# Optimization experiments

Hardware: AMD Instinct MI355X
Metric: run time of the kernel (lower is better)

The kernel has to match this reference:

```python
import jax, jax.numpy as jnp
import numpy as np

IN_FEATURES = 512
OUT_FEATURES = 256
N = 2048

def setup_inputs() -> dict:
    key = jax.random.key(0)
    k1, k2, k3 = jax.random.split(key, 3)
    x = jax.random.normal(k1, (N, IN_FEATURES), dtype=jnp.float32)
    # kaiming_uniform_(a=sqrt(5)) -> uniform(-b, b) with b = sqrt(6/((1+5)*fan_in)) = 1/sqrt(fan_in)
    bound_w = 1.0 / np.sqrt(IN_FEATURES)
    weight = jax.random.uniform(k2, (OUT_FEATURES, IN_FEATURES), dtype=jnp.float32,
                                minval=-bound_w, maxval=bound_w)
    bound_b = 1.0 / np.sqrt(IN_FEATURES)
    bias = jax.random.uniform(k3, (OUT_FEATURES,), dtype=jnp.float32,
                              minval=-bound_b, maxval=bound_b)
    return {"x": x, "weight": weight, "bias": bias}

def reference(x, weight, bias):
    # MAM fully-connected (beta == 0 path):
    # prod[n, k, j] = x[n, k] * weight[j, k]
    # C[n, j] = max_k prod[n,k,j] + min_k prod[n,k,j] + bias[j]
    prod = x[:, :, None] * weight.T[None, :, :]   # [N, in, out]
    C = jnp.max(prod, axis=1) + jnp.min(prod, axis=1) + bias[None, :]
    return C
```

## Files before the change

kernel.cpp:

```cpp
#include <hip/hip_runtime.h>
#include <math.h>

#define N_ 2048
#define K_ 512
#define J_ 256
#define KC 64
#define NPW 16

typedef float f32x16 __attribute__((ext_vector_type(16)));

#define MAX3(acc, a, b) asm("v_max3_f32 %0, %0, %1, %2" : "+v"(acc) : "v"(a), "v"(b))
#define MIN3(acc, a, b) asm("v_min3_f32 %0, %0, %1, %2" : "+v"(acc) : "v"(a), "v"(b))

__global__ __launch_bounds__(512, 4) void mam_fused5(
    const float* __restrict__ x, const float* __restrict__ w,
    const float* __restrict__ bias, float* __restrict__ out)
{
    __shared__ float cmb[8][NPW][128];

    const int t    = threadIdx.x;
    const int lane = t & 63;
    const int kc   = __builtin_amdgcn_readfirstlane(t >> 6);

    const int wg0 = (int)blockIdx.x;
    const int wg  = (wg0 & 7) * 64 + (wg0 >> 3);
    const int jb  = wg & 3;
    const int ng  = wg >> 2;

    const int j   = jb * 64 + lane;
    const int n0  = ng * NPW;

    float4 wreg[16];
    {
        const float4* wp = (const float4*)(w + (size_t)j * K_ + kc * KC);
#pragma unroll
        for (int i = 0; i < 16; ++i) wreg[i] = wp[i];
    }

    const float* xb = x + (size_t)n0 * K_ + kc * KC;

    float mxv[NPW], mnv[NPW];
#pragma unroll
    for (int n = 0; n < NPW; ++n) { mxv[n] = -__builtin_inff(); mnv[n] = __builtin_inff(); }

#pragma unroll
    for (int n = 0; n < NPW; ++n) {
        f32x16 xv[4];
        asm volatile(
            "s_load_dwordx16 %0, %4, %5\n\t"
            "s_load_dwordx16 %1, %4, %6\n\t"
            "s_load_dwordx16 %2, %4, %7\n\t"
            "s_load_dwordx16 %3, %4, %8\n\t"
            "s_waitcnt lgkmcnt(0)"
            : "=&s"(xv[0]), "=&s"(xv[1]), "=&s"(xv[2]), "=&s"(xv[3])
            : "s"(xb), "i"(n * 2048 + 0), "i"(n * 2048 + 64),
              "i"(n * 2048 + 128), "i"(n * 2048 + 192));
#pragma unroll
        for (int i = 0; i < 16; ++i) {
            const float p0 = wreg[i].x * xv[i >> 2][(i & 3) * 4 + 0];
            const float p1 = wreg[i].y * xv[i >> 2][(i & 3) * 4 + 1];
            const float p2 = wreg[i].z * xv[i >> 2][(i & 3) * 4 + 2];
            const float p3 = wreg[i].w * xv[i >> 2][(i & 3) * 4 + 3];
            MAX3(mxv[n], p0, p1); MAX3(mxv[n], p2, p3);
            MIN3(mnv[n], p0, p1); MIN3(mnv[n], p2, p3);
        }
    }

#pragma unroll
    for (int n = 0; n < NPW; ++n) {
        cmb[kc][n][lane]      = mxv[n];
        cmb[kc][n][64 + lane] = mnv[n];
    }
    __syncthreads();

    const float bj = bias[j];
#pragma unroll
    for (int u = 0; u < 2; ++u) {
        const int n = kc * 2 + u;
        float a = cmb[0][n][lane];
        float b = cmb[0][n][64 + lane];
#pragma unroll
        for (int c = 1; c < 8; ++c) {
            a = fmaxf(a, cmb[c][n][lane]);
            b = fminf(b, cmb[c][n][64 + lane]);
        }
        out[(size_t)(n0 + n) * J_ + j] = a + b + bj;
    }
}

extern "C" void kernel_launch(void* const* d_in, const int* in_sizes, int n_in,
                              void* d_out, int out_size, void* d_ws, size_t ws_size,
                              hipStream_t stream) {
    const float* x    = (const float*)d_in[0];
    const float* w    = (const float*)d_in[1];
    const float* bias = (const float*)d_in[2];
    float* out = (float*)d_out;

    dim3 grid(512);
    mam_fused5<<<grid, 512, 0, stream>>>(x, w, bias, out);
}
```

Baseline: 73.90 us.

## Retile so each block covers all outputs for 4 rows, staging x in LDS

Each block now handles 4 rows of x and all 256 output columns. Each wave owns a 64-wide K slice and streams the weights from global in 8-column sub-chunks, while the x rows are staged into LDS through direct global-to-LDS loads. This replaces the earlier 16-row by 64-column tiling that held weights in registers and read x through scalar loads. The weights are now reread from global/L2 by every block, and each weight load waits on vmcnt(0) before computing, which may expose latency. The LDS reduction buffer also grows to 64KB, which may limit occupancy.

```diff
diff --git a/kernel.cpp b/kernel.cpp
--- a/kernel.cpp
+++ b/kernel.cpp
@@ -4,87 +4,119 @@
 #define N_ 2048
 #define K_ 512
 #define J_ 256
-#define KC 64
-#define NPW 16
+#define NR 4
 
-typedef float f32x16 __attribute__((ext_vector_type(16)));
+typedef __attribute__((address_space(3))) float       lds_f;
+typedef const __attribute__((address_space(1))) float glb_f;
 
 #define MAX3(acc, a, b) asm("v_max3_f32 %0, %0, %1, %2" : "+v"(acc) : "v"(a), "v"(b))
 #define MIN3(acc, a, b) asm("v_min3_f32 %0, %0, %1, %2" : "+v"(acc) : "v"(a), "v"(b))
 
-__global__ __launch_bounds__(512, 4) void mam_fused5(
+__global__ __launch_bounds__(512, 4) void mam_fused7(
     const float* __restrict__ x, const float* __restrict__ w,
     const float* __restrict__ bias, float* __restrict__ out)
 {
-    __shared__ float cmb[8][NPW][128];
+    __shared__ __align__(16) float xls[NR * 512];
+    __shared__ __align__(16) float cmb[8 * NR * J_ * 2];
 
     const int t    = threadIdx.x;
     const int lane = t & 63;
     const int kc   = __builtin_amdgcn_readfirstlane(t >> 6);
+    const int n0   = (int)blockIdx.x * NR;
 
-    const int wg0 = (int)blockIdx.x;
-    const int wg  = (wg0 & 7) * 64 + (wg0 >> 3);
-    const int jb  = wg & 3;
-    const int ng  = wg >> 2;
-
-    const int j   = jb * 64 + lane;
-    const int n0  = ng * NPW;
-
-    float4 wreg[16];
     {
-        const float4* wp = (const float4*)(w + (size_t)j * K_ + kc * KC);
-#pragma unroll
-        for (int i = 0; i < 16; ++i) wreg[i] = wp[i];
+        const int r = kc >> 1, h = kc & 1;
+        __builtin_amdgcn_global_load_lds(
+            (glb_f*)(x + (size_t)(n0 + r) * K_ + h * 256 + lane * 4),
+            (lds_f*)(xls + r * 512 + h * 256), 16, 0, 0);
     }
 
-    const float* xb = x + (size_t)n0 * K_ + kc * KC;
+    const float* wq[4];
+#pragma unroll
+    for (int q = 0; q < 4; ++q)
+        wq[q] = w + (size_t)(q * 64 + lane) * K_ + kc * 64;
 
-    float mxv[NPW], mnv[NPW];
+    float mx[NR][4], mn[NR][4];
 #pragma unroll
-    for (int n = 0; n < NPW; ++n) { mxv[n] = -__builtin_inff(); mnv[n] = __builtin_inff(); }
+    for (int n = 0; n < NR; ++n)
+#pragma unroll
+        for (int q = 0; q < 4; ++q) {
+            mx[n][q] = -__builtin_inff();
+            mn[n][q] =  __builtin_inff();
+        }
+
+    __syncthreads();
+
+    float4 wv[4][2];
+
+#define WLOAD(S0, S1)                                                         \
+    asm volatile(                                                             \
+        "global_load_dwordx4 %0, %8, off offset:" S0 "\n\t"                   \
+        "global_load_dwordx4 %1, %8, off offset:" S1 "\n\t"                   \
+        "global_load_dwordx4 %2, %9, off offset:" S0 "\n\t"                   \
+        "global_load_dwordx4 %3, %9, off offset:" S1 "\n\t"                   \
+        "global_load_dwordx4 %4, %10, off offset:" S0 "\n\t"                  \
+        "global_load_dwordx4 %5, %10, off offset:" S1 "\n\t"                  \
+        "global_load_dwordx4 %6, %11, off offset:" S0 "\n\t"                  \
+        "global_load_dwordx4 %7, %11, off offset:" S1 "\n\t"                  \
+        "s_waitcnt vmcnt(0)"                                                  \
+        : "=&v"(wv[0][0]), "=&v"(wv[0][1]), "=&v"(wv[1][0]), "=&v"(wv[1][1]), \
+          "=&v"(wv[2][0]), "=&v"(wv[2][1]), "=&v"(wv[3][0]), "=&v"(wv[3][1])  \
+        : "v"(wq[0]), "v"(wq[1]), "v"(wq[2]), "v"(wq[3]))
+
+#define CSUB(S)                                                               \
+    _Pragma("unroll")                                                         \
+    for (int n = 0; n < NR; ++n) {                                            \
+        const float4 x0 = *(const float4*)&xls[n * 512 + kc * 64 + (S) * 8];  \
+        const float4 x1 = *(const float4*)&xls[n * 512 + kc * 64 + (S) * 8 + 4]; \
+        _Pragma("unroll")                                                     \
+        for (int q = 0; q < 4; ++q) {                                         \
+            const float4 a0 = wv[q][0], a1 = wv[q][1];                        \
+            const float p0 = x0.x * a0.x, p1 = x0.y * a0.y;                   \
+            const float p2 = x0.z * a0.z, p3 = x0.w * a0.w;                   \
+            const float p4 = x1.x * a1.x, p5 = x1.y * a1.y;                   \
+            const float p6 = x1.z * a1.z, p7 = x1.w * a1.w;                   \
+            MAX3(mx[n][q], p0, p1); MAX3(mx[n][q], p2, p3);                   \
+            MAX3(mx[n][q], p4, p5); MAX3(mx[n][q], p6, p7);                   \
+            MIN3(mn[n][q], p0, p1); MIN3(mn[n][q], p2, p3);                   \
+            MIN3(mn[n][q], p4, p5); MIN3(mn[n][q], p6, p7);                   \
+        }                                                                     \
+    }
+
+    WLOAD(  "0",  "16"); CSUB(0);
+    WLOAD( "32",  "48"); CSUB(1);
+    WLOAD( "64",  "80"); CSUB(2);
+    WLOAD( "96", "112"); CSUB(3);
+    WLOAD("128", "144"); CSUB(4);
+    WLOAD("160", "176"); CSUB(5);
+    WLOAD("192", "208"); CSUB(6);
+    WLOAD("224", "240"); CSUB(7);
+
+#undef WLOAD
+#undef CSUB
 
 #pragma unroll
-    for (int n = 0; n < NPW; ++n) {
-        f32x16 xv[4];
-        asm volatile(
-            "s_load_dwordx16 %0, %4, %5\n\t"
-            "s_load_dwordx16 %1, %4, %6\n\t"
-            "s_load_dwordx16 %2, %4, %7\n\t"
-            "s_load_dwordx16 %3, %4, %8\n\t"
-            "s_waitcnt lgkmcnt(0)"
-            : "=&s"(xv[0]), "=&s"(xv[1]), "=&s"(xv[2]), "=&s"(xv[3])
-            : "s"(xb), "i"(n * 2048 + 0), "i"(n * 2048 + 64),
-              "i"(n * 2048 + 128), "i"(n * 2048 + 192));
+    for (int n = 0; n < NR; ++n)
 #pragma unroll
-        for (int i = 0; i < 16; ++i) {
-            const float p0 = wreg[i].x * xv[i >> 2][(i & 3) * 4 + 0];
-            const float p1 = wreg[i].y * xv[i >> 2][(i & 3) * 4 + 1];
-            const float p2 = wreg[i].z * xv[i >> 2][(i & 3) * 4 + 2];
-            const float p3 = wreg[i].w * xv[i >> 2][(i & 3) * 4 + 3];
-            MAX3(mxv[n], p0, p1); MAX3(mxv[n], p2, p3);
-            MIN3(mnv[n], p0, p1); MIN3(mnv[n], p2, p3);
+        for (int q = 0; q < 4; ++q) {
+            float2 v; v.x = mx[n][q]; v.y = mn[n][q];
+            *(float2*)&cmb[((kc * NR + n) * J_ + q * 64 + lane) * 2] = v;
         }
-    }
+    __syncthreads();
 
 #pragma unroll
-    for (int n = 0; n < NPW; ++n) {
-        cmb[kc][n][lane]      = mxv[n];
-        cmb[kc][n][64 + lane] = mnv[n];
-    }
-    __syncthreads();
-
-    const float bj = bias[j];
+    for (int i = 0; i < 2; ++i) {
+        const int u = t + i * 512;
+        const int n = u >> 8;
+        const int j = u & 255;
+        float a = -__builtin_inff(), b = __builtin_inff();
 #pragma unroll
-    for (int u = 0; u < 2; ++u) {
-        const int n = kc * 2 + u;
-        float a = cmb[0][n][lane];
-        float b = cmb[0][n][64 + lane];
-#pragma unroll
-        for (int c = 1; c < 8; ++c) {
-            a = fmaxf(a, cmb[c][n][lane]);
-            b = fminf(b, cmb[c][n][64 + lane]);
+        for (int c = 0; c < 8; ++c) {
+            const float2 p = *(const float2*)&cmb[((c * NR + n) * J_ + j) * 2];
+            a = fmaxf(a, p.x);
+            b = fminf(b, p.y);
         }
-        out[(size_t)(n0 + n) * J_ + j] = a + b + bj;
+        out[(size_t)(n0 + n) * J_ + j] = a + b + bias[j];
     }
 }
 
@@ -96,6 +128,6 @@
     const float* bias = (const float*)d_in[2];
     float* out = (float*)d_out;
 
-    dim3 grid(512);
-    mam_fused5<<<grid, 512, 0, stream>>>(x, w, bias, out);
+    dim3 grid(N_ / NR);
+    mam_fused7<<<grid, 512, 0, stream>>>(x, w, bias, out);
 }
```

Result: slower. 91.91 us (+24.4%).

## Retile max-min FC into 64x8 LDS register blocks with staged global loads

Applied to the files above, without the earlier changes.

Replaces the per-wave scalar-load scheme (each lane holds one weight column and streams x rows through SGPRs) with a 64-row by 8-column output tile per block. Four waves each handle a 128-wide K slice, staging x and w chunks through padded LDS, and each lane computes a 4x2 register tile. The next chunk's global loads are issued before the current chunk's compute to overlap latency. This trades SGPR broadcast loads for LDS reads with 2D register reuse and changes the grid to 1024 blocks of 256 threads. The risks are LDS bandwidth and bank-conflict cost, and WRITES overwriting LDS that other lanes may still be reading, since each wave appears to touch only its own region.

```diff
diff --git a/kernel.cpp b/kernel.cpp
--- a/kernel.cpp
+++ b/kernel.cpp
@@ -4,87 +4,143 @@
 #define N_ 2048
 #define K_ 512
 #define J_ 256
-#define KC 64
-#define NPW 16
 
-typedef float f32x16 __attribute__((ext_vector_type(16)));
+typedef float f32x4 __attribute__((ext_vector_type(4)));
+typedef float f32x2 __attribute__((ext_vector_type(2)));
+typedef __attribute__((address_space(3))) float  lds_f;
+typedef __attribute__((address_space(3))) f32x4  lds_f4;
 
 #define MAX3(acc, a, b) asm("v_max3_f32 %0, %0, %1, %2" : "+v"(acc) : "v"(a), "v"(b))
 #define MIN3(acc, a, b) asm("v_min3_f32 %0, %0, %1, %2" : "+v"(acc) : "v"(a), "v"(b))
 
-__global__ __launch_bounds__(512, 4) void mam_fused5(
+__global__ __launch_bounds__(256, 4) void mam_fused8(
     const float* __restrict__ x, const float* __restrict__ w,
     const float* __restrict__ bias, float* __restrict__ out)
 {
-    __shared__ float cmb[8][NPW][128];
+    __shared__ __align__(16) float sm[9856];
 
     const int t    = threadIdx.x;
     const int lane = t & 63;
-    const int kc   = __builtin_amdgcn_readfirstlane(t >> 6);
+    const int ks   = __builtin_amdgcn_readfirstlane(t >> 6);
 
     const int wg0 = (int)blockIdx.x;
-    const int wg  = (wg0 & 7) * 64 + (wg0 >> 3);
-    const int jb  = wg & 3;
-    const int ng  = wg >> 2;
+    const int wg  = (wg0 & 7) * 128 + (wg0 >> 3);
+    const int bx  = wg & 31;
+    const int by  = wg >> 5;
+    const int j0  = bx * 8;
+    const int n0  = by * 64;
 
-    const int j   = jb * 64 + lane;
-    const int n0  = ng * NPW;
+    const int rg = lane >> 2;
+    const int cg = lane & 3;
 
-    float4 wreg[16];
-    {
-        const float4* wp = (const float4*)(w + (size_t)j * K_ + kc * KC);
+    const int XB = ks * 2176;
+    const int WB = 8704 + ks * 288;
+
+    const float* xsb = x + (size_t)n0 * K_ + ks * 128;
+    const float* wsb = w + (size_t)j0 * K_ + ks * 128;
+
+    unsigned vxo[8];
 #pragma unroll
-        for (int i = 0; i < 16; ++i) wreg[i] = wp[i];
+    for (int m = 0; m < 8; ++m)
+        vxo[m] = (unsigned)((lane >> 3) * 2048 + (lane & 7) * 16 + m * 16384);
+    const unsigned vwo = (unsigned)((lane >> 3) * 2048 + (lane & 7) * 16);
+
+    lds_f* xwp = (lds_f*)&sm[XB] + (lane >> 4) * 68 + ((lane >> 3) & 1) * 32 + (lane & 7) * 4;
+    lds_f* wwp = (lds_f*)&sm[WB] + (lane >> 3) * 36 + (lane & 7) * 4;
+
+    float mx[4][2], mn[4][2];
+#pragma unroll
+    for (int i = 0; i < 4; ++i)
+#pragma unroll
+        for (int jj = 0; jj < 2; ++jj) {
+            mx[i][jj] = -__builtin_inff();
+            mn[i][jj] =  __builtin_inff();
+        }
+
+    f32x4 px[8], pw;
+
+#define LOADS(OFS)                                                            \
+    asm volatile(                                                             \
+        "global_load_dwordx4 %0, %9, %17 offset:" OFS "\n\t"                  \
+        "global_load_dwordx4 %1, %10, %17 offset:" OFS "\n\t"                 \
+        "global_load_dwordx4 %2, %11, %17 offset:" OFS "\n\t"                 \
+        "global_load_dwordx4 %3, %12, %17 offset:" OFS "\n\t"                 \
+        "global_load_dwordx4 %4, %13, %17 offset:" OFS "\n\t"                 \
+        "global_load_dwordx4 %5, %14, %17 offset:" OFS "\n\t"                 \
+        "global_load_dwordx4 %6, %15, %17 offset:" OFS "\n\t"                 \
+        "global_load_dwordx4 %7, %16, %17 offset:" OFS "\n\t"                 \
+        "global_load_dwordx4 %8, %18, %19 offset:" OFS                        \
+        : "=&v"(px[0]), "=&v"(px[1]), "=&v"(px[2]), "=&v"(px[3]),             \
+          "=&v"(px[4]), "=&v"(px[5]), "=&v"(px[6]), "=&v"(px[7]), "=&v"(pw)   \
+        : "v"(vxo[0]), "v"(vxo[1]), "v"(vxo[2]), "v"(vxo[3]),                 \
+          "v"(vxo[4]), "v"(vxo[5]), "v"(vxo[6]), "v"(vxo[7]),                 \
+          "s"(xsb), "v"(vwo), "s"(wsb))
+
+#define WRITES()                                                              \
+    {                                                                         \
+        asm volatile("s_waitcnt vmcnt(0)" ::: "memory");                      \
+        _Pragma("unroll")                                                     \
+        for (int m = 0; m < 8; ++m)                                           \
+            *(lds_f4*)(xwp + m * 272) = px[m];                                \
+        *(lds_f4*)wwp = pw;                                                   \
     }
 
-    const float* xb = x + (size_t)n0 * K_ + kc * KC;
+#define COMPUTE()                                                             \
+    _Pragma("unroll")                                                         \
+    for (int q = 0; q < 8; ++q) {                                             \
+        f32x4 xv[4], wv[2];                                                   \
+        _Pragma("unroll")                                                     \
+        for (int i = 0; i < 4; ++i)                                           \
+            xv[i] = *(const f32x4*)&sm[XB + ((rg >> 1) + 8 * i) * 68          \
+                                       + (rg & 1) * 32 + q * 4];              \
+        _Pragma("unroll")                                                     \
+        for (int jj = 0; jj < 2; ++jj)                                        \
+            wv[jj] = *(const f32x4*)&sm[WB + (cg * 2 + jj) * 36 + q * 4];     \
+        _Pragma("unroll")                                                     \
+        for (int i = 0; i < 4; ++i)                                           \
+            _Pragma("unroll")                                                 \
+            for (int jj = 0; jj < 2; ++jj) {                                  \
+                const f32x4 a = xv[i], b = wv[jj];                            \
+                const float p0 = a.x * b.x, p1 = a.y * b.y;                   \
+                const float p2 = a.z * b.z, p3 = a.w * b.w;                   \
+                MAX3(mx[i][jj], p0, p1); MAX3(mx[i][jj], p2, p3);             \
+                MIN3(mn[i][jj], p0, p1); MIN3(mn[i][jj], p2, p3);             \
+            }                                                                 \
+    }
 
-    float mxv[NPW], mnv[NPW];
+    LOADS("0");   WRITES();
+    LOADS("128"); COMPUTE(); WRITES();
+    LOADS("256"); COMPUTE(); WRITES();
+    LOADS("384"); COMPUTE(); WRITES();
+    COMPUTE();
+
+#undef LOADS
+#undef WRITES
+#undef COMPUTE
+
+    __syncthreads();
 #pragma unroll
-    for (int n = 0; n < NPW; ++n) { mxv[n] = -__builtin_inff(); mnv[n] = __builtin_inff(); }
+    for (int i = 0; i < 4; ++i)
+#pragma unroll
+        for (int jj = 0; jj < 2; ++jj) {
+            const int o = (rg + 16 * i) * 8 + cg * 2 + jj;
+            f32x2 v; v.x = mx[i][jj]; v.y = mn[i][jj];
+            *(f32x2*)&sm[(ks * 512 + o) * 2] = v;
+        }
+    __syncthreads();
 
 #pragma unroll
-    for (int n = 0; n < NPW; ++n) {
-        f32x16 xv[4];
-        asm volatile(
-            "s_load_dwordx16 %0, %4, %5\n\t"
-            "s_load_dwordx16 %1, %4, %6\n\t"
-            "s_load_dwordx16 %2, %4, %7\n\t"
-            "s_load_dwordx16 %3, %4, %8\n\t"
-            "s_waitcnt lgkmcnt(0)"
-            : "=&s"(xv[0]), "=&s"(xv[1]), "=&s"(xv[2]), "=&s"(xv[3])
-            : "s"(xb), "i"(n * 2048 + 0), "i"(n * 2048 + 64),
-              "i"(n * 2048 + 128), "i"(n * 2048 + 192));
+    for (int e = 0; e < 2; ++e) {
+        const int o = t + e * 256;
+        float a = -__builtin_inff(), b = __builtin_inff();
 #pragma unroll
-        for (int i = 0; i < 16; ++i) {
-            const float p0 = wreg[i].x * xv[i >> 2][(i & 3) * 4 + 0];
-            const float p1 = wreg[i].y * xv[i >> 2][(i & 3) * 4 + 1];
-            const float p2 = wreg[i].z * xv[i >> 2][(i & 3) * 4 + 2];
-            const float p3 = wreg[i].w * xv[i >> 2][(i & 3) * 4 + 3];
-            MAX3(mxv[n], p0, p1); MAX3(mxv[n], p2, p3);
-            MIN3(mnv[n], p0, p1); MIN3(mnv[n], p2, p3);
+        for (int s = 0; s < 4; ++s) {
+            const f32x2 p = *(const f32x2*)&sm[(s * 512 + o) * 2];
+            a = fmaxf(a, p.x);
+            b = fminf(b, p.y);
         }
-    }
-
-#pragma unroll
-    for (int n = 0; n < NPW; ++n) {
-        cmb[kc][n][lane]      = mxv[n];
-        cmb[kc][n][64 + lane] = mnv[n];
-    }
-    __syncthreads();
-
-    const float bj = bias[j];
-#pragma unroll
-    for (int u = 0; u < 2; ++u) {
-        const int n = kc * 2 + u;
-        float a = cmb[0][n][lane];
-        float b = cmb[0][n][64 + lane];
-#pragma unroll
-        for (int c = 1; c < 8; ++c) {
-            a = fmaxf(a, cmb[c][n][lane]);
-            b = fminf(b, cmb[c][n][64 + lane]);
-        }
-        out[(size_t)(n0 + n) * J_ + j] = a + b + bj;
+        const int r = o >> 3, c = o & 7;
+        out[(size_t)(n0 + r) * J_ + j0 + c] = a + b + bias[j0 + c];
     }
 }
 
@@ -96,6 +152,6 @@
     const float* bias = (const float*)d_in[2];
     float* out = (float*)d_out;
 
-    dim3 grid(512);
-    mam_fused5<<<grid, 512, 0, stream>>>(x, w, bias, out);
+    dim3 grid(1024);
+    mam_fused8<<<grid, 256, 0, stream>>>(x, w, bias, out);
 }
```

New measurement: 72.69 us. About the same (-1.6%).
